# Performance work log

Hardware: AMD Instinct MI355X
Metric: run time of the kernel (lower is better)

## Reference

```python
import jax, jax.numpy as jnp
import numpy as np

EMBED = 1024
HEADS = 16
HEAD_SIZE = EMBED // HEADS


def setup_inputs() -> dict:
    key = jax.random.key(0)
    ks = jax.random.split(key, 11)
    B, S, E = 2, 2048, EMBED
    scale = 1.0 / np.sqrt(E)
    return {
        'q': jax.random.normal(ks[0], (B, S, E), jnp.float32),
        'k': jax.random.normal(ks[1], (B, S, E), jnp.float32),
        'v': jax.random.normal(ks[2], (B, S, E), jnp.float32),
        'Wq': jax.random.normal(ks[3], (E, E), jnp.float32) * scale,
        'bq': jnp.zeros((E,), jnp.float32),
        'Wk': jax.random.normal(ks[4], (E, E), jnp.float32) * scale,
        'bk': jnp.zeros((E,), jnp.float32),
        'Wv': jax.random.normal(ks[5], (E, E), jnp.float32) * scale,
        'bv': jnp.zeros((E,), jnp.float32),
        'Wo': jax.random.normal(ks[6], (E, E), jnp.float32) * scale,
        'bo': jnp.zeros((E,), jnp.float32),
    }


def reference(q, k, v, Wq, bq, Wk, bk, Wv, bv, Wo, bo):
    B, Sq, E = q.shape
    Sk = k.shape[1]
    # linear projections (torch Linear: x @ W.T + b), split into heads
    qh = (q @ Wq.T + bq).reshape(B, Sq, HEADS, HEAD_SIZE)
    kh = (k @ Wk.T + bk).reshape(B, Sk, HEADS, HEAD_SIZE)
    vh = (v @ Wv.T + bv).reshape(B, Sk, HEADS, HEAD_SIZE)
    # NOTE: original scales by 1/sqrt(embed_size), not head_size
    scores = jnp.einsum('bqhe,bkhe->bhqk', qh, kh) / jnp.sqrt(jnp.float32(E))
    probs = jax.nn.softmax(scores, axis=-1)  # dropout eval-mode: identity
    attn = jnp.einsum('bhqk,bkhd->bqhd', probs, vh)
    out = attn.reshape(B, Sq, E) @ Wo.T + bo
    return out
```

## Files before the change

kernel.cpp:

```cpp
#include <hip/hip_runtime.h>


typedef unsigned short u16;
typedef __bf16 bf16x8 __attribute__((ext_vector_type(8)));
typedef float f32x4 __attribute__((ext_vector_type(4)));
typedef u16 u16x4 __attribute__((ext_vector_type(4)));
typedef u16 u16x8 __attribute__((ext_vector_type(8)));

typedef __attribute__((address_space(1))) const unsigned int as1_cu32;
typedef __attribute__((address_space(3))) unsigned int as3_u32;

#if __has_builtin(__builtin_amdgcn_exp2f)
#define EXP2(x) __builtin_amdgcn_exp2f(x)
#else
#define EXP2(x) exp2f(x)
#endif

__device__ __forceinline__ u16 f2bf(float f) {
  unsigned u = __builtin_bit_cast(unsigned, f);
  u += 0x7fffu + ((u >> 16) & 1u);
  return (u16)(u >> 16);
}

__device__ __forceinline__ void gl_lds16(const u16* g, u16* l) {
  __builtin_amdgcn_global_load_lds((as1_cu32*)g, (as3_u32*)l, 16, 0, 0);
}

__global__ void cast_kernel(const float* __restrict__ q, const float* __restrict__ k,
                            const float* __restrict__ v, const float* __restrict__ wq,
                            const float* __restrict__ wk, const float* __restrict__ wv,
                            const float* __restrict__ wo,
                            u16* __restrict__ qb, u16* __restrict__ kb, u16* __restrict__ vb,
                            u16* __restrict__ wqb, u16* __restrict__ wkb, u16* __restrict__ wvb,
                            u16* __restrict__ wob) {
  unsigned t = blockIdx.x * 256u + threadIdx.x;
  const float* src; u16* dst; unsigned off;
  if (t < 3u * 1048576u) {
    unsigned which = t >> 20;
    off = t & 1048575u;
    src = which == 0 ? q : (which == 1 ? k : v);
    dst = which == 0 ? qb : (which == 1 ? kb : vb);
  } else {
    unsigned tw = t - 3u * 1048576u;
    unsigned which = tw >> 18;
    off = tw & 262143u;
    src = which == 0 ? wq : (which == 1 ? wk : (which == 2 ? wv : wo));
    dst = which == 0 ? wqb : (which == 1 ? wkb : (which == 2 ? wvb : wob));
  }
  float4 f = ((const float4*)src)[off];
  u16x4 o;
  o[0] = f2bf(f.x); o[1] = f2bf(f.y); o[2] = f2bf(f.z); o[3] = f2bf(f.w);
  ((u16x4*)dst)[off] = o;
}

template <int BM>
__device__ __forceinline__ void gemm_stage(const u16* A, const u16* B,
                                           u16 (&As)[BM][32], u16 (&Bs)[128][32],
                                           int m0, int n0, int kt, int w, int l) {
#pragma unroll
  for (int i = 0; i < BM / 64; ++i) {
    int r0 = i * 64 + w * 16;
    gl_lds16(A + (size_t)(m0 + r0 + (l >> 2)) * 1024 + kt * 32 + (l & 3) * 8, &As[r0][0]);
  }
#pragma unroll
  for (int i = 0; i < 2; ++i) {
    int r0 = i * 64 + w * 16;
    gl_lds16(B + (size_t)(n0 + r0 + (l >> 2)) * 1024 + kt * 32 + (l & 3) * 8, &Bs[r0][0]);
  }
}

template <int MODE, int BM>
__device__ __forceinline__ void gemm_body(const u16* __restrict__ A, const u16* __restrict__ B,
                                          const float* __restrict__ bias, void* __restrict__ Cv,
                                          float scale, char* SMraw) {
  constexpr int MI = BM / 32;
  u16 (*Asp)[BM][32] = (u16(*)[BM][32])SMraw;
  u16 (*Bsp)[128][32] = (u16(*)[128][32])(SMraw + BM * 128);
  constexpr int N = 1024, NK = 32;
  const int m0 = blockIdx.x * BM;
  const int n0 = blockIdx.y * 128;
  const int tid = threadIdx.x;
  const int w = tid >> 6, l = tid & 63;
  const int lr = l & 15, lg = l >> 4;
  const int wm = (w >> 1) * (BM / 2), wn = (w & 1) * 64;

  f32x4 acc[MI][4];
#pragma unroll
  for (int i = 0; i < MI; ++i)
#pragma unroll
    for (int j = 0; j < 4; ++j) acc[i][j] = f32x4{0.f, 0.f, 0.f, 0.f};

  gemm_stage<BM>(A, B, Asp[0], Bsp[0], m0, n0, 0, w, l);

  for (int kt = 0; kt < NK; ++kt) {
    const int buf = kt & 1;
    __syncthreads();
    if (kt + 1 < NK) gemm_stage<BM>(A, B, Asp[buf ^ 1], Bsp[buf ^ 1], m0, n0, kt + 1, w, l);
    bf16x8 af[MI], bfr[4];
#pragma unroll
    for (int i = 0; i < MI; ++i)
      af[i] = *(const bf16x8*)&Asp[buf][wm + i * 16 + lr][lg * 8];
#pragma unroll
    for (int i = 0; i < 4; ++i)
      bfr[i] = *(const bf16x8*)&Bsp[buf][wn + i * 16 + lr][lg * 8];
#pragma unroll
    for (int mi = 0; mi < MI; ++mi)
#pragma unroll
      for (int ni = 0; ni < 4; ++ni)
        acc[mi][ni] = __builtin_amdgcn_mfma_f32_16x16x32_bf16(af[mi], bfr[ni], acc[mi][ni], 0, 0, 0);
  }

  float bv[4];
#pragma unroll
  for (int ni = 0; ni < 4; ++ni) bv[ni] = bias[n0 + wn + ni * 16 + lr];

  if constexpr (MODE != 2) {
#pragma unroll
    for (int mi = 0; mi < MI; ++mi)
#pragma unroll
      for (int ni = 0; ni < 4; ++ni)
#pragma unroll
        for (int r = 0; r < 4; ++r) {
          const int row = m0 + wm + mi * 16 + lg * 4 + r;
          const int col = n0 + wn + ni * 16 + lr;
          float vv = (acc[mi][ni][r] + bv[ni]) * scale;
          if constexpr (MODE == 1) ((float*)Cv)[(size_t)row * N + col] = vv;
          else                     ((u16*)Cv)[(size_t)row * N + col] = f2bf(vv);
        }
  } else {
    __syncthreads();
    char* wb = SMraw + w * 8192;
#pragma unroll
    for (int mi = 0; mi < MI; ++mi)
#pragma unroll
      for (int ni = 0; ni < 4; ++ni)
#pragma unroll
        for (int r = 0; r < 4; ++r) {
          const int dl = ni * 16 + lr;
          const int sl = mi * 16 + lg * 4 + r;
          const int phys = (sl >> 3) ^ (lr & 7);
          *(u16*)(wb + dl * 128 + (phys << 4) + (sl & 7) * 2) =
              f2bf(acc[mi][ni][r] + bv[ni]);
        }
    const int sc2 = l & 7, srl2 = l >> 3;
    const int rowg = m0 + wm;
#pragma unroll
    for (int i = 0; i < 8; ++i) {
      const int dl = i * 8 + srl2;
      const int phys = sc2 ^ srl2;
      u16x8 vrow = *(u16x8*)(wb + dl * 128 + (phys << 4));
      const int colg = n0 + wn + dl;
      u16* dst = (u16*)Cv + ((size_t)((rowg >> 11) << 10) + colg) * 2048 +
                 (rowg & 2047) + sc2 * 8;
      *(u16x8*)dst = vrow;
    }
  }
}

__global__ __launch_bounds__(256, 2)
void proj_kernel(const u16* __restrict__ qb, const u16* __restrict__ kb, const u16* __restrict__ vb,
                 const u16* __restrict__ wqb, const u16* __restrict__ wkb, const u16* __restrict__ wvb,
                 const float* __restrict__ bq, const float* __restrict__ bk, const float* __restrict__ bvv,
                 u16* __restrict__ qh, u16* __restrict__ kh, u16* __restrict__ vt) {
  __shared__ __align__(16) char SM[32768];
  if (blockIdx.z == 0)      gemm_body<0, 128>(qb, wqb, bq, qh, 1.44269504089f / 32.f, SM);
  else if (blockIdx.z == 1) gemm_body<0, 128>(kb, wkb, bk, kh, 1.0f, SM);
  else                      gemm_body<2, 128>(vb, wvb, bvv, vt, 1.0f, SM);
}

__global__ __launch_bounds__(256, 2)
void outproj_kernel(const u16* __restrict__ attnb, const u16* __restrict__ wob,
                    const float* __restrict__ bo, float* __restrict__ out) {
  __shared__ __align__(16) char SM[24576];
  gemm_body<1, 64>(attnb, wob, bo, out, 1.0f, SM);
}

__global__ __launch_bounds__(256, 2)
void attn_kernel(const u16* __restrict__ Q, const u16* __restrict__ Kh,
                 const u16* __restrict__ Vt, u16* __restrict__ Ao) {
  constexpr int E = 1024, S = 2048, NT = S / 64;
  const int bh = blockIdx.x, qt = blockIdx.y;
  const int b = bh >> 4, h = bh & 15;
  const int tid = threadIdx.x, w = tid >> 6, l = tid & 63;
  const int lr = l & 15, lg = l >> 4;

  __shared__ __align__(16) char SM[32768];

  const u16* Qp = Q + (size_t)b * S * E + (size_t)h * 64;
  const u16* Kp = Kh + (size_t)b * S * E + (size_t)h * 64;
  const u16* Vp = Vt + (size_t)bh * 64 * S;

  const int qbase = qt * 128 + w * 32;
  bf16x8 qa[2][2];
#pragma unroll
  for (int qh = 0; qh < 2; ++qh)
#pragma unroll
    for (int hh = 0; hh < 2; ++hh)
      qa[qh][hh] = *(const bf16x8*)(Qp + (size_t)(qbase + qh * 16 + lr) * E + hh * 32 + lg * 8);

  bf16x8 ones;
#pragma unroll
  for (int j = 0; j < 8; ++j) ones[j] = (__bf16)1.0f;

  f32x4 o_acc[2][4];
#pragma unroll
  for (int qh = 0; qh < 2; ++qh)
#pragma unroll
    for (int nf = 0; nf < 4; ++nf) o_acc[qh][nf] = f32x4{0.f, 0.f, 0.f, 0.f};
  f32x4 sum_acc[2] = {f32x4{0.f, 0.f, 0.f, 0.f}, f32x4{0.f, 0.f, 0.f, 0.f}};

  const int swz8 = lr & 7;
  int fofs0[4], fofs1[4];
#pragma unroll
  for (int nf = 0; nf < 4; ++nf) {
    fofs0[nf] = (((nf * 16 + lr) * 64) + (lg ^ swz8) * 8) * 2;
    fofs1[nf] = (((nf * 16 + lr) * 64) + ((4 + lg) ^ swz8) * 8) * 2;
  }

  const int sc = l & 7, srl = l >> 3;
  auto kperm = [](int r) {
    return (r & 35) | ((r & 12) << 1) | ((r & 16) >> 2);
  };
  auto stageK = [&](int buf, int kb) {
#pragma unroll
    for (int i = 0; i < 2; ++i) {
      const int row = i * 32 + w * 8 + srl;
      const int cp = sc ^ (row & 7);
      gl_lds16(Kp + (size_t)(kb + kperm(row)) * E + cp * 8,
               (u16*)(SM + buf * 8192 + (i * 32 + w * 8) * 128));
    }
  };
  auto stageV = [&](int buf, int kb) {
#pragma unroll
    for (int i = 0; i < 2; ++i) {
      const int row = i * 32 + w * 8 + srl;
      const int cp = sc ^ (row & 7);
      gl_lds16(Vp + (size_t)row * S + kb + cp * 8,
               (u16*)(SM + 16384 + buf * 8192 + (i * 32 + w * 8) * 128));
    }
  };

  stageK(0, 0); stageV(0, 0);
  for (int t = 0; t < NT; ++t) {
    const int cur = t & 1;
    __syncthreads();
    if (t + 1 < NT) { stageK(cur ^ 1, (t + 1) * 64); stageV(cur ^ 1, (t + 1) * 64); }
    const char* Kc = SM + cur * 8192;
    const char* Vc = SM + 16384 + cur * 8192;

    f32x4 sfr[2][4];
    __builtin_amdgcn_s_setprio(1);
#pragma unroll
    for (int nf = 0; nf < 4; ++nf) {
      bf16x8 k0 = *(const bf16x8*)(Kc + fofs0[nf]);
      bf16x8 k1 = *(const bf16x8*)(Kc + fofs1[nf]);
#pragma unroll
      for (int qh = 0; qh < 2; ++qh) {
        f32x4 z = f32x4{0.f, 0.f, 0.f, 0.f};
        z = __builtin_amdgcn_mfma_f32_16x16x32_bf16(k0, qa[qh][0], z, 0, 0, 0);
        sfr[qh][nf] = __builtin_amdgcn_mfma_f32_16x16x32_bf16(k1, qa[qh][1], z, 0, 0, 0);
      }
    }
    __builtin_amdgcn_s_setprio(0);

    bf16x8 pa0[2], pa1[2];
#pragma unroll
    for (int qh = 0; qh < 2; ++qh)
#pragma unroll
      for (int r = 0; r < 4; ++r) {
        pa0[qh][r]     = (__bf16)EXP2(sfr[qh][0][r]);
        pa0[qh][4 + r] = (__bf16)EXP2(sfr[qh][1][r]);
        pa1[qh][r]     = (__bf16)EXP2(sfr[qh][2][r]);
        pa1[qh][4 + r] = (__bf16)EXP2(sfr[qh][3][r]);
      }

#pragma unroll
    for (int qh = 0; qh < 2; ++qh) {
      sum_acc[qh] = __builtin_amdgcn_mfma_f32_16x16x32_bf16(pa0[qh], ones, sum_acc[qh], 0, 0, 0);
      sum_acc[qh] = __builtin_amdgcn_mfma_f32_16x16x32_bf16(pa1[qh], ones, sum_acc[qh], 0, 0, 0);
    }

    __builtin_amdgcn_s_setprio(1);
#pragma unroll
    for (int nf = 0; nf < 4; ++nf) {
      bf16x8 vb0 = *(const bf16x8*)(Vc + fofs0[nf]);
      bf16x8 vb1 = *(const bf16x8*)(Vc + fofs1[nf]);
#pragma unroll
      for (int qh = 0; qh < 2; ++qh) {
        o_acc[qh][nf] = __builtin_amdgcn_mfma_f32_16x16x32_bf16(pa0[qh], vb0, o_acc[qh][nf], 0, 0, 0);
        o_acc[qh][nf] = __builtin_amdgcn_mfma_f32_16x16x32_bf16(pa1[qh], vb1, o_acc[qh][nf], 0, 0, 0);
      }
    }
    __builtin_amdgcn_s_setprio(0);
  }

#pragma unroll
  for (int qh = 0; qh < 2; ++qh)
#pragma unroll
    for (int r = 0; r < 4; ++r) {
      const float inv = 1.0f / sum_acc[qh][r];
      const size_t row = (size_t)b * S + qbase + qh * 16 + lg * 4 + r;
#pragma unroll
      for (int nf = 0; nf < 4; ++nf)
        Ao[row * E + h * 64 + nf * 16 + lr] = f2bf(o_acc[qh][nf][r] * inv);
    }
}

extern "C" void kernel_launch(void* const* d_in, const int* in_sizes, int n_in,
                              void* d_out, int out_size, void* d_ws, size_t ws_size,
                              hipStream_t stream) {
  const float* q  = (const float*)d_in[0];
  const float* k  = (const float*)d_in[1];
  const float* v  = (const float*)d_in[2];
  const float* Wq = (const float*)d_in[3];
  const float* bq = (const float*)d_in[4];
  const float* Wk = (const float*)d_in[5];
  const float* bk = (const float*)d_in[6];
  const float* Wv = (const float*)d_in[7];
  const float* bv = (const float*)d_in[8];
  const float* Wo = (const float*)d_in[9];
  const float* bo = (const float*)d_in[10];
  float* out = (float*)d_out;

  char* ws = (char*)d_ws;
  u16* qb  = (u16*)(ws);
  u16* kb  = (u16*)(ws + (8u << 20));
  u16* vb  = (u16*)(ws + (16u << 20));
  u16* wqb = (u16*)(ws + (24u << 20));
  u16* wkb = (u16*)(ws + (26u << 20));
  u16* wvb = (u16*)(ws + (28u << 20));
  u16* wob = (u16*)(ws + (30u << 20));
  u16* qhp = (u16*)(ws + (32u << 20));
  u16* khp = (u16*)(ws + (40u << 20));
  u16* vtp = (u16*)(ws + (48u << 20));
  u16* attnb = qb;

  cast_kernel<<<dim3(16384), dim3(256), 0, stream>>>(q, k, v, Wq, Wk, Wv, Wo,
                                                     qb, kb, vb, wqb, wkb, wvb, wob);
  proj_kernel<<<dim3(32, 8, 3), dim3(256), 0, stream>>>(qb, kb, vb, wqb, wkb, wvb,
                                                        bq, bk, bv, qhp, khp, vtp);
  attn_kernel<<<dim3(32, 16), dim3(256), 0, stream>>>(qhp, khp, vtp, attnb);
  outproj_kernel<<<dim3(64, 8), dim3(256), 0, stream>>>(attnb, wob, bo, out);
}
```

Measured before the change: 107.5 us.

## Fuse activation fp32-to-bf16 cast into projection GEMM tile loads

Removes the activation cast pass and has the projection GEMM load fp32 q/k/v tiles directly into LDS with an XOR swizzle, converting to bf16 when forming MFMA fragments. This eliminates writing and rereading bf16 copies of the activations and shrinks the cast kernel to weights only. In exchange the projection kernel moves twice the A bytes per tile, uses more LDS (48KB), and does conversion work in the inner loop, which may reduce occupancy or add VALU pressure.

```diff
diff --git a/kernel.cpp b/kernel.cpp
--- a/kernel.cpp
+++ b/kernel.cpp
@@ -26,56 +26,28 @@
   __builtin_amdgcn_global_load_lds((as1_cu32*)g, (as3_u32*)l, 16, 0, 0);
 }
 
-__global__ void cast_kernel(const float* __restrict__ q, const float* __restrict__ k,
-                            const float* __restrict__ v, const float* __restrict__ wq,
-                            const float* __restrict__ wk, const float* __restrict__ wv,
-                            const float* __restrict__ wo,
-                            u16* __restrict__ qb, u16* __restrict__ kb, u16* __restrict__ vb,
-                            u16* __restrict__ wqb, u16* __restrict__ wkb, u16* __restrict__ wvb,
-                            u16* __restrict__ wob) {
+__global__ void cast_kernel(const float* __restrict__ wq, const float* __restrict__ wk,
+                            const float* __restrict__ wv, const float* __restrict__ wo,
+                            u16* __restrict__ wqb, u16* __restrict__ wkb,
+                            u16* __restrict__ wvb, u16* __restrict__ wob) {
   unsigned t = blockIdx.x * 256u + threadIdx.x;
-  const float* src; u16* dst; unsigned off;
-  if (t < 3u * 1048576u) {
-    unsigned which = t >> 20;
-    off = t & 1048575u;
-    src = which == 0 ? q : (which == 1 ? k : v);
-    dst = which == 0 ? qb : (which == 1 ? kb : vb);
-  } else {
-    unsigned tw = t - 3u * 1048576u;
-    unsigned which = tw >> 18;
-    off = tw & 262143u;
-    src = which == 0 ? wq : (which == 1 ? wk : (which == 2 ? wv : wo));
-    dst = which == 0 ? wqb : (which == 1 ? wkb : (which == 2 ? wvb : wob));
-  }
+  unsigned which = t >> 18, off = t & 262143u;
+  const float* src = which == 0 ? wq : (which == 1 ? wk : (which == 2 ? wv : wo));
+  u16* dst = which == 0 ? wqb : (which == 1 ? wkb : (which == 2 ? wvb : wob));
   float4 f = ((const float4*)src)[off];
   u16x4 o;
   o[0] = f2bf(f.x); o[1] = f2bf(f.y); o[2] = f2bf(f.z); o[3] = f2bf(f.w);
   ((u16x4*)dst)[off] = o;
 }
 
-template <int BM>
-__device__ __forceinline__ void gemm_stage(const u16* A, const u16* B,
-                                           u16 (&As)[BM][32], u16 (&Bs)[128][32],
-                                           int m0, int n0, int kt, int w, int l) {
-#pragma unroll
-  for (int i = 0; i < BM / 64; ++i) {
-    int r0 = i * 64 + w * 16;
-    gl_lds16(A + (size_t)(m0 + r0 + (l >> 2)) * 1024 + kt * 32 + (l & 3) * 8, &As[r0][0]);
-  }
-#pragma unroll
-  for (int i = 0; i < 2; ++i) {
-    int r0 = i * 64 + w * 16;
-    gl_lds16(B + (size_t)(n0 + r0 + (l >> 2)) * 1024 + kt * 32 + (l & 3) * 8, &Bs[r0][0]);
-  }
-}
-
-template <int MODE, int BM>
-__device__ __forceinline__ void gemm_body(const u16* __restrict__ A, const u16* __restrict__ B,
+template <int MODE, int BM, bool AF32>
+__device__ __forceinline__ void gemm_body(const void* __restrict__ Av, const u16* __restrict__ B,
                                           const float* __restrict__ bias, void* __restrict__ Cv,
                                           float scale, char* SMraw) {
   constexpr int MI = BM / 32;
-  u16 (*Asp)[BM][32] = (u16(*)[BM][32])SMraw;
-  u16 (*Bsp)[128][32] = (u16(*)[128][32])(SMraw + BM * 128);
+  constexpr int ABUF = AF32 ? (BM * 128) : (BM * 64);
+  char* ASM = SMraw;
+  char* BSM = SMraw + 2 * ABUF;
   constexpr int N = 1024, NK = 32;
   const int m0 = blockIdx.x * BM;
   const int n0 = blockIdx.y * 128;
@@ -84,25 +56,65 @@
   const int lr = l & 15, lg = l >> 4;
   const int wm = (w >> 1) * (BM / 2), wn = (w & 1) * 64;
 
+  auto stage = [&](int buf, int kt) {
+    if constexpr (AF32) {
+      const float* A = (const float*)Av;
+#pragma unroll
+      for (int i = 0; i < BM / 32; ++i) {
+        const int row = i * 32 + w * 8 + (l >> 3);
+        const int cp = (l & 7) ^ (row & 7);
+        gl_lds16((const u16*)(A + (size_t)(m0 + row) * 1024 + kt * 32 + cp * 4),
+                 (u16*)(ASM + buf * ABUF + (i * 32 + w * 8) * 128));
+      }
+    } else {
+      const u16* A = (const u16*)Av;
+#pragma unroll
+      for (int i = 0; i < BM / 64; ++i) {
+        const int r0 = i * 64 + w * 16;
+        gl_lds16(A + (size_t)(m0 + r0 + (l >> 2)) * 1024 + kt * 32 + (l & 3) * 8,
+                 (u16*)(ASM + buf * ABUF + r0 * 64));
+      }
+    }
+#pragma unroll
+    for (int i = 0; i < 2; ++i) {
+      const int r0 = i * 64 + w * 16;
+      gl_lds16(B + (size_t)(n0 + r0 + (l >> 2)) * 1024 + kt * 32 + (l & 3) * 8,
+               (u16*)(BSM + buf * 8192 + r0 * 64));
+    }
+  };
+
   f32x4 acc[MI][4];
 #pragma unroll
   for (int i = 0; i < MI; ++i)
 #pragma unroll
     for (int j = 0; j < 4; ++j) acc[i][j] = f32x4{0.f, 0.f, 0.f, 0.f};
 
-  gemm_stage<BM>(A, B, Asp[0], Bsp[0], m0, n0, 0, w, l);
+  stage(0, 0);
 
   for (int kt = 0; kt < NK; ++kt) {
     const int buf = kt & 1;
     __syncthreads();
-    if (kt + 1 < NK) gemm_stage<BM>(A, B, Asp[buf ^ 1], Bsp[buf ^ 1], m0, n0, kt + 1, w, l);
+    if (kt + 1 < NK) stage(buf ^ 1, kt + 1);
     bf16x8 af[MI], bfr[4];
-#pragma unroll
-    for (int i = 0; i < MI; ++i)
-      af[i] = *(const bf16x8*)&Asp[buf][wm + i * 16 + lr][lg * 8];
+    if constexpr (AF32) {
+      const char* Ab = ASM + buf * ABUF;
+#pragma unroll
+      for (int i = 0; i < MI; ++i) {
+        const int arow = wm + i * 16 + lr;
+        const char* base = Ab + arow * 128;
+        f32x4 a0 = *(const f32x4*)(base + (((lg * 2) ^ (arow & 7)) << 4));
+        f32x4 a1 = *(const f32x4*)(base + (((lg * 2 + 1) ^ (arow & 7)) << 4));
+#pragma unroll
+        for (int j = 0; j < 4; ++j) { af[i][j] = (__bf16)a0[j]; af[i][4 + j] = (__bf16)a1[j]; }
+      }
+    } else {
+#pragma unroll
+      for (int i = 0; i < MI; ++i)
+        af[i] = *(const bf16x8*)(ASM + buf * ABUF + (wm + i * 16 + lr) * 64 + lg * 16);
+    }
 #pragma unroll
     for (int i = 0; i < 4; ++i)
-      bfr[i] = *(const bf16x8*)&Bsp[buf][wn + i * 16 + lr][lg * 8];
+      bfr[i] = *(const bf16x8*)(BSM + buf * 8192 + (wn + i * 16 + lr) * 64 + lg * 16);
 #pragma unroll
     for (int mi = 0; mi < MI; ++mi)
 #pragma unroll
@@ -158,21 +170,21 @@
 }
 
 __global__ __launch_bounds__(256, 2)
-void proj_kernel(const u16* __restrict__ qb, const u16* __restrict__ kb, const u16* __restrict__ vb,
+void proj_kernel(const float* __restrict__ q, const float* __restrict__ k, const float* __restrict__ v,
                  const u16* __restrict__ wqb, const u16* __restrict__ wkb, const u16* __restrict__ wvb,
                  const float* __restrict__ bq, const float* __restrict__ bk, const float* __restrict__ bvv,
                  u16* __restrict__ qh, u16* __restrict__ kh, u16* __restrict__ vt) {
-  __shared__ __align__(16) char SM[32768];
-  if (blockIdx.z == 0)      gemm_body<0, 128>(qb, wqb, bq, qh, 1.44269504089f / 32.f, SM);
-  else if (blockIdx.z == 1) gemm_body<0, 128>(kb, wkb, bk, kh, 1.0f, SM);
-  else                      gemm_body<2, 128>(vb, wvb, bvv, vt, 1.0f, SM);
+  __shared__ __align__(16) char SM[49152];
+  if (blockIdx.z == 0)      gemm_body<0, 128, true>(q, wqb, bq, qh, 1.44269504089f / 32.f, SM);
+  else if (blockIdx.z == 1) gemm_body<0, 128, true>(k, wkb, bk, kh, 1.0f, SM);
+  else                      gemm_body<2, 128, true>(v, wvb, bvv, vt, 1.0f, SM);
 }
 
 __global__ __launch_bounds__(256, 2)
 void outproj_kernel(const u16* __restrict__ attnb, const u16* __restrict__ wob,
                     const float* __restrict__ bo, float* __restrict__ out) {
   __shared__ __align__(16) char SM[24576];
-  gemm_body<1, 64>(attnb, wob, bo, out, 1.0f, SM);
+  gemm_body<1, 64, false>(attnb, wob, bo, out, 1.0f, SM);
 }
 
 __global__ __launch_bounds__(256, 2)
@@ -323,9 +335,7 @@
   float* out = (float*)d_out;
 
   char* ws = (char*)d_ws;
-  u16* qb  = (u16*)(ws);
-  u16* kb  = (u16*)(ws + (8u << 20));
-  u16* vb  = (u16*)(ws + (16u << 20));
+  u16* attnb = (u16*)(ws);
   u16* wqb = (u16*)(ws + (24u << 20));
   u16* wkb = (u16*)(ws + (26u << 20));
   u16* wvb = (u16*)(ws + (28u << 20));
@@ -333,11 +343,9 @@
   u16* qhp = (u16*)(ws + (32u << 20));
   u16* khp = (u16*)(ws + (40u << 20));
   u16* vtp = (u16*)(ws + (48u << 20));
-  u16* attnb = qb;
-
-  cast_kernel<<<dim3(16384), dim3(256), 0, stream>>>(q, k, v, Wq, Wk, Wv, Wo,
-                                                     qb, kb, vb, wqb, wkb, wvb, wob);
-  proj_kernel<<<dim3(32, 8, 3), dim3(256), 0, stream>>>(qb, kb, vb, wqb, wkb, wvb,
+
+  cast_kernel<<<dim3(4096), dim3(256), 0, stream>>>(Wq, Wk, Wv, Wo, wqb, wkb, wvb, wob);
+  proj_kernel<<<dim3(32, 8, 3), dim3(256), 0, stream>>>(q, k, v, wqb, wkb, wvb,
                                                         bq, bk, bv, qhp, khp, vtp);
   attn_kernel<<<dim3(32, 16), dim3(256), 0, stream>>>(qhp, khp, vtp, attnb);
   outproj_kernel<<<dim3(64, 8), dim3(256), 0, stream>>>(attnb, wob, bo, out);
```

Result: faster. 105.3 us (-2.1%).
